# Kernel tuning notes

Measured on AMD Instinct MI355X. Metric: run time of the kernel, lower is better.

Reference implementation:

```python
import jax, jax.numpy as jnp
from jax import lax
import numpy as np

# ---- static configuration (RPN inference path) ----
B = 8
IMG_H, IMG_W = 800, 1216
LEVEL_GRIDS = [(200, 304), (100, 152), (50, 76), (25, 38), (13, 19)]
STRIDES = [4, 8, 16, 32, 64]
SIZES = [32, 64, 128, 256, 512]
RATIOS = np.array([0.5, 1.0, 2.0])
NUM_PER_LEVEL = [h * w * 3 for (h, w) in LEVEL_GRIDS]  # [182400,45600,11400,2850,741]
A_TOTAL = sum(NUM_PER_LEVEL)                            # 242991
PRE_N = 1000   # pre_nms_top_n['testing'], applied per level
POST_N = 1000  # post_nms_top_n['testing']
NMS_THRESH = 0.7
SCORE_THRESH = 0.0
MIN_SIZE = 0.001
BBOX_XFORM_CLIP = float(np.log(1000.0 / 16.0))
LEVEL_OFFSET = 4096.0  # > max image coord, for batched_nms level separation

K_PER_LEVEL = [min(PRE_N, n) for n in NUM_PER_LEVEL]
K_TOTAL = sum(K_PER_LEVEL)  # 4741
LEVELS = jnp.concatenate([jnp.full((k,), i, dtype=jnp.int32)
                          for i, k in enumerate(K_PER_LEVEL)])


def _make_anchors():
    """torchvision-style grid anchors, one scale + 3 aspect ratios per level."""
    all_anchors = []
    for (fh, fw), stride, size in zip(LEVEL_GRIDS, STRIDES, SIZES):
        h_ratios = np.sqrt(RATIOS)
        w_ratios = 1.0 / h_ratios
        ws = w_ratios * size
        hs = h_ratios * size
        base = np.stack([-ws / 2, -hs / 2, ws / 2, hs / 2], axis=1)  # [3,4]
        sx = np.arange(fw, dtype=np.float32) * stride
        sy = np.arange(fh, dtype=np.float32) * stride
        yy, xx = np.meshgrid(sy, sx, indexing='ij')
        shifts = np.stack([xx, yy, xx, yy], axis=-1).reshape(-1, 1, 4)  # [fh*fw,1,4]
        anchors = (shifts + base[None]).reshape(-1, 4)                  # [fh*fw*3,4]
        all_anchors.append(anchors.astype(np.float32))
    return np.concatenate(all_anchors, axis=0)  # [A_TOTAL,4]


def setup_inputs() -> dict:
    key = jax.random.key(0)
    k1, k2 = jax.random.split(key)
    objectness = jax.random.normal(k1, (B, A_TOTAL), dtype=jnp.float32)
    pred_bbox_deltas = jax.random.normal(k2, (B, A_TOTAL, 4), dtype=jnp.float32) * 0.5
    anchors = jnp.asarray(_make_anchors())
    return {"objectness": objectness, "pred_bbox_deltas": pred_bbox_deltas,
            "anchors": anchors}


def _decode(deltas, anchors):
    """BoxCoder.decode with weights (1,1,1,1). deltas [B,A,4], anchors [A,4]."""
    wa = anchors[:, 2] - anchors[:, 0]
    ha = anchors[:, 3] - anchors[:, 1]
    cxa = anchors[:, 0] + 0.5 * wa
    cya = anchors[:, 1] + 0.5 * ha
    dx, dy, dw, dh = deltas[..., 0], deltas[..., 1], deltas[..., 2], deltas[..., 3]
    dw = jnp.minimum(dw, BBOX_XFORM_CLIP)
    dh = jnp.minimum(dh, BBOX_XFORM_CLIP)
    cx = dx * wa + cxa
    cy = dy * ha + cya
    w = jnp.exp(dw) * wa
    h = jnp.exp(dh) * ha
    return jnp.stack([cx - 0.5 * w, cy - 0.5 * h, cx + 0.5 * w, cy + 0.5 * h], axis=-1)


def _per_level_topk(objectness):
    """_get_top_n_idx: per-level top-k with global offsets. Returns [B,K_TOTAL] int32."""
    idxs, offset = [], 0
    for n, k in zip(NUM_PER_LEVEL, K_PER_LEVEL):
        _, ti = lax.top_k(objectness[:, offset:offset + n], k)
        idxs.append(ti + offset)
        offset += n
    return jnp.concatenate(idxs, axis=1)


def _iou(boxes):  # boxes [K,4] -> [K,K]
    area = (boxes[:, 2] - boxes[:, 0]) * (boxes[:, 3] - boxes[:, 1])
    lt = jnp.maximum(boxes[:, None, :2], boxes[None, :, :2])
    rb = jnp.minimum(boxes[:, None, 2:], boxes[None, :, 2:])
    wh = jnp.clip(rb - lt, 0.0)
    inter = wh[..., 0] * wh[..., 1]
    return inter / (area[:, None] + area[None, :] - inter)


def _nms_image(boxes, scores, levels, valid):
    """clip->filter->batched_nms->post_nms_top_n for one image (fixed shapes)."""
    K = boxes.shape[0]
    order = jnp.argsort(-jnp.where(valid, scores, -jnp.inf))
    b = boxes[order]
    s = scores[order]
    v = valid[order]
    lv = levels[order]
    # batched NMS: offset boxes by level so cross-level boxes never overlap
    bb = b + lv.astype(b.dtype)[:, None] * LEVEL_OFFSET
    iou = lax.stop_gradient(_iou(bb))  # keep decisions are non-differentiable
    idxr = jnp.arange(K)

    def body(i, keep):
        sup = (iou[i] > NMS_THRESH) & (idxr > i) & keep[i]
        return keep & ~sup

    keep = lax.fori_loop(0, K, body, v)
    sel = jnp.where(keep, s, -1.0)  # sigmoid scores are > 0
    top_s, top_i = lax.top_k(sel, POST_N)
    kept = top_s > 0.0
    out_b = jnp.where(kept[:, None], b[top_i], 0.0)
    out_s = jnp.where(kept, top_s, 0.0)
    return out_b, out_s


def reference(objectness, pred_bbox_deltas, anchors):
    # box decode for all anchors
    proposals = _decode(pred_bbox_deltas, anchors)          # [B,A,4]
    # per-level topk + gather
    idx = _per_level_topk(objectness)                       # [B,K]
    obj = jnp.take_along_axis(objectness, idx, axis=1)      # [B,K]
    props = jnp.take_along_axis(proposals, idx[..., None], axis=1)  # [B,K,4]
    scores = jax.nn.sigmoid(obj)
    lv = jnp.broadcast_to(LEVELS, idx.shape)
    # clip_boxes_to_image
    x1 = jnp.clip(props[..., 0], 0.0, IMG_W)
    y1 = jnp.clip(props[..., 1], 0.0, IMG_H)
    x2 = jnp.clip(props[..., 2], 0.0, IMG_W)
    y2 = jnp.clip(props[..., 3], 0.0, IMG_H)
    props = jnp.stack([x1, y1, x2, y2], axis=-1)
    # remove_small_boxes + score_thresh
    valid = (x2 - x1 >= MIN_SIZE) & (y2 - y1 >= MIN_SIZE) & (scores >= SCORE_THRESH)
    boxes_out, scores_out = jax.vmap(_nms_image)(props, scores, lv, valid)
    return boxes_out, scores_out  # [B,POST_N,4], [B,POST_N] (zero-padded)
```

## Files before the change

### kernel.cpp

```cpp
#include <hip/hip_runtime.h>
#include <stdint.h>

#pragma clang fp contract(off)

typedef unsigned int u32;
typedef unsigned long long u64;

#define A_TOTAL 242991
#define KTOT    4741

__constant__ int c_LN[5]   = {182400, 45600, 11400, 2850, 741};
__constant__ int c_LOFF[5] = {0, 182400, 228000, 239400, 242250};
__constant__ int c_LK[5]   = {1000, 1000, 1000, 1000, 741};

__constant__ int c_SL[33] = {0,0,0,0,0,0,0,0,0,0,0,0,0,0,0,0,0,0,0,0,0,0,0,
                             1,1,1,1,1,1, 2,2, 3, 4};
__constant__ int c_SS[33] = {0,8192,16384,24576,32768,40960,49152,57344,65536,
                             73728,81920,90112,98304,106496,114688,122880,131072,
                             139264,147456,155648,163840,172032,180224,
                             0,8192,16384,24576,32768,40960, 0,8192, 0, 0};

__constant__ int c_MW[40] = {0,1,2,3, 4,4, 5,5, 6,6, 7,7, 8,8,8, 9,9,9,
                             10,10,10, 11,11,11, 12,12,12,12, 13,13,13,13,
                             14,14,14,14, 15,15,15,15};
__constant__ int c_MR[40] = {0,0,0,0, 0,1, 0,1, 0,1, 0,1, 0,1,2, 0,1,2,
                             0,1,2, 0,1,2, 0,1,2,3, 0,1,2,3,
                             0,1,2,3, 0,1,2,3};

static const size_t OFF_KEEPW    = 0;
static const size_t OFF_HIST     = 0;
static const size_t OFF_SELCNT   = 327680;
static const size_t OFF_CANDCNT  = 327840;
static const size_t MEMSET_BYTES = 328000;
static const size_t OFF_TBIN     = 328000;
static const size_t OFF_CLESS    = 328160;
static const size_t OFF_SELG     = 328320;
static const size_t OFF_CANDG    = 656000;
static const size_t OFF_KEYS     = 1966720;
static const size_t OFF_BOX      = 2270144;
static const size_t OFF_SCORE    = 2876992;
static const size_t OFF_VALID    = 3028704;
static const size_t OFF_MASK     = 3180416;
static const size_t OFF_OUTK     = 8423296;

__device__ __forceinline__ u32 fmap(float f){
  u32 b = __float_as_uint(f);
  return (b & 0x80000000u) ? ~b : (b | 0x80000000u);
}
__device__ __forceinline__ float funmap(u32 m){
  return __uint_as_float((m & 0x80000000u) ? (m & 0x7FFFFFFFu) : ~m);
}

__global__ void __launch_bounds__(1024)
k_hist(const float* __restrict__ obj, u32* __restrict__ hist)
{
  int b = blockIdx.x / 33, s = blockIdx.x % 33;
  int l = c_SL[s], start = c_SS[s];
  int cnt = c_LN[l] - start; if (cnt > 8192) cnt = 8192;
  int bl = b * 5 + l;
  __shared__ u32 h[4][2048];
  for (int i = threadIdx.x; i < 8192; i += 1024) ((u32*)h)[i] = 0;
  __syncthreads();
  u32* hw = h[(threadIdx.x >> 6) & 3];
  const float* p = obj + (size_t)b * A_TOTAL + c_LOFF[l] + start;
  int head = (4 - (int)(((size_t)p >> 2) & 3)) & 3;
  if (head > cnt) head = cnt;
  if ((int)threadIdx.x < head) atomicAdd(&hw[(~fmap(p[threadIdx.x])) >> 21], 1u);
  int nvec = (cnt - head) >> 2;
  const float4* pv = (const float4*)(p + head);
  for (int i = threadIdx.x; i < nvec; i += 1024){
    float4 v = pv[i];
    atomicAdd(&hw[(~fmap(v.x)) >> 21], 1u);
    atomicAdd(&hw[(~fmap(v.y)) >> 21], 1u);
    atomicAdd(&hw[(~fmap(v.z)) >> 21], 1u);
    atomicAdd(&hw[(~fmap(v.w)) >> 21], 1u);
  }
  int tail0 = head + (nvec << 2);
  int ntail = cnt - tail0;
  if ((int)threadIdx.x < ntail) atomicAdd(&hw[(~fmap(p[tail0 + threadIdx.x])) >> 21], 1u);
  __syncthreads();
  for (int i = threadIdx.x; i < 2048; i += 1024){
    u32 v = h[0][i] + h[1][i] + h[2][i] + h[3][i];
    if (v) atomicAdd(&hist[bl * 2048 + i], v);
  }
}

__global__ void __launch_bounds__(256)
k_cutoff(u32* __restrict__ hist, u32* __restrict__ tbin, u32* __restrict__ cless)
{
  int bl = blockIdx.x; int l = bl % 5;
  int K = c_LK[l], n = c_LN[l];
  int tid = threadIdx.x;
  __shared__ u32 cum[2048];
  __shared__ u32 part[256];
  __shared__ int s_t;
  u32 vals[8]; u32 sum = 0;
  for (int q = 0; q < 8; ++q){ vals[q] = hist[bl * 2048 + tid * 8 + q]; sum += vals[q]; }
  part[tid] = sum;
  __syncthreads();
  for (int off = 1; off < 256; off <<= 1){
    u32 add = (tid >= off) ? part[tid - off] : 0u;
    __syncthreads();
    part[tid] += add;
    __syncthreads();
  }
  u32 run = (tid > 0) ? part[tid - 1] : 0u;
  for (int q = 0; q < 8; ++q){ run += vals[q]; cum[tid * 8 + q] = run; }
  __syncthreads();
  if (K >= n){ if (tid == 0){ tbin[bl] = 2048u; cless[bl] = (u32)n; } return; }
  if (tid == 0) s_t = 0;
  __syncthreads();
  for (int q = 0; q < 8; ++q){
    int i = tid * 8 + q;
    u32 c = cum[i], cp = (i > 0) ? cum[i - 1] : 0u;
    if (c >= (u32)K && cp < (u32)K) s_t = i;
  }
  __syncthreads();
  if (tid == 0){
    int t = s_t;
    tbin[bl] = (u32)t;
    cless[bl] = (t > 0) ? cum[t - 1] : 0u;
  }
}

#define SELCAP 2048
#define CANDCAP 1024
__global__ void __launch_bounds__(1024)
k_collect(const float* __restrict__ obj, const u32* __restrict__ tbin,
          u32* __restrict__ selcnt, u32* __restrict__ candcnt,
          u64* __restrict__ selg, u64* __restrict__ candg)
{
  int b = blockIdx.x / 33, s = blockIdx.x % 33;
  int l = c_SL[s], start = c_SS[s];
  int cnt = c_LN[l] - start; if (cnt > 8192) cnt = 8192;
  int bl = b * 5 + l;
  u32 t = tbin[bl];
  __shared__ u64 lsel[SELCAP];
  __shared__ u64 lcand[CANDCAP];
  __shared__ u32 lcs, lcc, gbs, gbc;
  if (threadIdx.x == 0){ lcs = 0u; lcc = 0u; }
  __syncthreads();
  const float* p = obj + (size_t)b * A_TOTAL + c_LOFF[l] + start;

  auto push = [&](u32 m, int idx){
    u32 bin = m >> 21;
    u64 key = ((u64)m << 32) | (u32)idx;
    if (bin < t){
      u32 pos = atomicAdd(&lcs, 1u);
      if (pos < SELCAP) lsel[pos] = key;
      else { u32 gp = atomicAdd(&selcnt[bl], 1u); selg[(size_t)bl * 1024 + gp] = key; }
    } else if (bin == t){
      u32 pos = atomicAdd(&lcc, 1u);
      if (pos < CANDCAP) lcand[pos] = key;
      else { u32 gp = atomicAdd(&candcnt[bl], 1u); if (gp < 4096u) candg[(size_t)bl * 4096 + gp] = key; }
    }
  };

  int head = (4 - (int)(((size_t)p >> 2) & 3)) & 3;
  if (head > cnt) head = cnt;
  if ((int)threadIdx.x < head) push(~fmap(p[threadIdx.x]), start + (int)threadIdx.x);
  int nvec = (cnt - head) >> 2;
  const float4* pv = (const float4*)(p + head);
  for (int i = threadIdx.x; i < nvec; i += 1024){
    float4 v = pv[i];
    int e = start + head + (i << 2);
    push(~fmap(v.x), e);
    push(~fmap(v.y), e + 1);
    push(~fmap(v.z), e + 2);
    push(~fmap(v.w), e + 3);
  }
  int tail0 = head + (nvec << 2);
  int ntail = cnt - tail0;
  if ((int)threadIdx.x < ntail) push(~fmap(p[tail0 + threadIdx.x]), start + tail0 + (int)threadIdx.x);
  __syncthreads();
  u32 ns = lcs;  if (ns > SELCAP) ns = SELCAP;
  u32 ncd = lcc; if (ncd > CANDCAP) ncd = CANDCAP;
  if (threadIdx.x == 0){
    gbs = ns  ? atomicAdd(&selcnt[bl],  ns)  : 0u;
    gbc = ncd ? atomicAdd(&candcnt[bl], ncd) : 0u;
  }
  __syncthreads();
  u32 bs = gbs, bc = gbc;
  for (u32 i = threadIdx.x; i < ns; i += 1024)
    selg[(size_t)bl * 1024 + bs + i] = lsel[i];
  for (u32 i = threadIdx.x; i < ncd; i += 1024){
    u32 gp = bc + i;
    if (gp < 4096u) candg[(size_t)bl * 4096 + gp] = lcand[i];
  }
}

__global__ void __launch_bounds__(1024)
k_select(const u32* __restrict__ selcnt, const u32* __restrict__ candcnt,
         const u64* __restrict__ selg, const u64* __restrict__ candg,
         u64* __restrict__ keys)
{
  int bl = blockIdx.x; int b = bl / 5, l = bl % 5;
  int K = c_LK[l];
  int tid = threadIdx.x;
  __shared__ __align__(16) u64 selU[1024];
  __shared__ __align__(16) u64 candU[4098];
  u32 ns = selcnt[bl]; if (ns > 1024u) ns = 1024u;
  u32 nc = candcnt[bl]; if (nc > 4096u) nc = 4096u;
  int R = K - (int)ns;
  selU[tid] = (tid < (int)ns) ? selg[(size_t)bl * 1024 + tid] : ~0ULL;
  for (u32 i = tid; i < nc; i += 1024) candU[i] = candg[(size_t)bl * 4096 + i];
  u32 nce = (nc + 1u) & ~1u;
  if (tid == 0 && nce > nc) candU[nc] = ~0ULL;
  __syncthreads();
  u64* kout = keys + (size_t)b * KTOT + l * 1000;
  if (tid < (int)ns){
    u64 key = selU[tid];
    u32 r = 0;
    #pragma unroll 8
    for (u32 j = 0; j < 1024; j += 2){
      ulonglong2 v = *reinterpret_cast<const ulonglong2*>(&selU[j]);
      r += (v.x < key) + (v.y < key);
    }
    kout[r] = key;
  }
  if (R > 0){
    for (u32 s = tid; s < nc; s += 1024){
      u64 key = candU[s];
      u32 r = 0;
      #pragma unroll 8
      for (u32 j = 0; j < nce; j += 2){
        ulonglong2 v = *reinterpret_cast<const ulonglong2*>(&candU[j]);
        r += (v.x < key) + (v.y < key);
      }
      if (r < (u32)R) kout[ns + r] = key;
    }
  }
}

__global__ void __launch_bounds__(256)
k_decode(const u64* __restrict__ keys, const float* __restrict__ deltas,
         const float* __restrict__ anchors, float* __restrict__ boxes,
         float* __restrict__ scores, u32* __restrict__ valid)
{
  int g = blockIdx.x * 256 + threadIdx.x;
  if (g >= 8 * KTOT) return;
  int b = g / KTOT, kpos = g % KTOT;
  int l = kpos / 1000; if (l > 4) l = 4;
  u64 key = keys[g];
  u32 idx = (u32)key;
  float o = funmap(~(u32)(key >> 32));
  int ai = c_LOFF[l] + (int)idx;
  const float* a = anchors + (size_t)ai * 4;
  const float* d = deltas + ((size_t)b * A_TOTAL + ai) * 4;
  float a0 = a[0], a1 = a[1], a2 = a[2], a3 = a[3];
  float wa = __fsub_rn(a2, a0), ha = __fsub_rn(a3, a1);
  float cxa = __fadd_rn(a0, __fmul_rn(0.5f, wa));
  float cya = __fadd_rn(a1, __fmul_rn(0.5f, ha));
  float dx = d[0], dy = d[1];
  float dw = fminf(d[2], 4.135166556742356f);
  float dh = fminf(d[3], 4.135166556742356f);
  float cx = __fadd_rn(__fmul_rn(dx, wa), cxa);
  float cy = __fadd_rn(__fmul_rn(dy, ha), cya);
  float w  = __fmul_rn(expf(dw), wa);
  float h  = __fmul_rn(expf(dh), ha);
  float hw = __fmul_rn(0.5f, w), hh = __fmul_rn(0.5f, h);
  float x1 = __fsub_rn(cx, hw), y1 = __fsub_rn(cy, hh);
  float x2 = __fadd_rn(cx, hw), y2 = __fadd_rn(cy, hh);
  x1 = fminf(fmaxf(x1, 0.0f), 1216.0f);
  x2 = fminf(fmaxf(x2, 0.0f), 1216.0f);
  y1 = fminf(fmaxf(y1, 0.0f), 800.0f);
  y2 = fminf(fmaxf(y2, 0.0f), 800.0f);
  float s = __fdiv_rn(1.0f, __fadd_rn(1.0f, expf(-o)));
  int v = (__fsub_rn(x2, x1) >= 0.001f) && (__fsub_rn(y2, y1) >= 0.001f) && (s >= 0.0f);
  float* bo = boxes + (size_t)g * 4;
  bo[0] = x1; bo[1] = y1; bo[2] = x2; bo[3] = y2;
  scores[g] = s;
  valid[g] = (u32)v;
}

__global__ void __launch_bounds__(256)
k_mask(const float* __restrict__ boxes, u64* __restrict__ mask)
{
  int b = blockIdx.x / 184, s = blockIdx.x % 184;
  int l, idx;
  if (s < 160){ l = s / 40; idx = s % 40; }
  else        { l = 4;      idx = s - 160; }
  int w = c_MW[idx], rb = c_MR[idx];
  int N = c_LK[l];
  int koff = l * 1000;
  float offv = (float)(l * 4096);
  __shared__ float sjx1[64], sjy1[64], sjx2[64], sjy2[64], sjar[64];
  int jbase = w * 64;
  if (threadIdx.x < 64){
    int j = jbase + (int)threadIdx.x;
    float x1, y1, x2, y2, ar;
    if (j < N){
      float4 p = ((const float4*)boxes)[(size_t)(b * KTOT + koff + j)];
      x1 = __fadd_rn(p.x, offv); y1 = __fadd_rn(p.y, offv);
      x2 = __fadd_rn(p.z, offv); y2 = __fadd_rn(p.w, offv);
      ar = __fmul_rn(__fsub_rn(x2, x1), __fsub_rn(y2, y1));
    } else {
      x1 = 3e38f; y1 = 3e38f; x2 = -3e38f; y2 = -3e38f; ar = 0.f;
    }
    sjx1[threadIdx.x] = x1; sjy1[threadIdx.x] = y1;
    sjx2[threadIdx.x] = x2; sjy2[threadIdx.x] = y2; sjar[threadIdx.x] = ar;
  }
  __syncthreads();
  int i = rb * 256 + (int)threadIdx.x;
  int rows = (w + 1) * 64; if (rows > N) rows = N;
  if (i >= rows) return;
  float4 p = ((const float4*)boxes)[(size_t)(b * KTOT + koff + i)];
  float bx1 = __fadd_rn(p.x, offv), by1 = __fadd_rn(p.y, offv);
  float bx2 = __fadd_rn(p.z, offv), by2 = __fadd_rn(p.w, offv);
  float bar = __fmul_rn(__fsub_rn(bx2, bx1), __fsub_rn(by2, by1));
  u64 bw = 0;
  #pragma unroll 16
  for (int jj = 0; jj < 64; ++jj){
    int j = jbase + jj;
    float ltx = fmaxf(bx1, sjx1[jj]), lty = fmaxf(by1, sjy1[jj]);
    float rbx = fminf(bx2, sjx2[jj]), rby = fminf(by2, sjy2[jj]);
    float wx = fmaxf(__fsub_rn(rbx, ltx), 0.0f);
    float wy = fmaxf(__fsub_rn(rby, lty), 0.0f);
    float inter = __fmul_rn(wx, wy);
    bool sup = false;
    if (inter > 0.0f && j > i){
      float den = __fsub_rn(__fadd_rn(bar, sjar[jj]), inter);
      sup = __fdiv_rn(inter, den) > 0.7f;
    }
    bw |= ((u64)sup) << jj;
  }
  mask[((size_t)(b * 5 + l) * 16 + w) * 1024 + i] = bw;
}

__global__ void __launch_bounds__(256)
k_nms(const u64* __restrict__ mask, const u32* __restrict__ valid,
      const float* __restrict__ scores, u64* __restrict__ outk,
      u64* __restrict__ keepw)
{
  int bl = blockIdx.x; int b = bl / 5, l = bl % 5;
  int N = c_LK[l], koff = l * 1000;
  int WN = (N + 63) >> 6;
  int tid = threadIdx.x;
  __shared__ u64 s_kw[16];
  __shared__ u64 s_m[7680];
  const u64* mb = mask + (size_t)bl * 16 * 1024;
  int wstage = (WN < 15) ? WN : 15;
  for (int w = 0; w < wstage; ++w){
    int rows = (w + 1) * 64;
    int base = 32 * w * (w + 1);
    for (int r = tid; r < rows; r += 256)
      s_m[base + r] = mb[(size_t)w * 1024 + r];
  }
  __syncthreads();
  if (tid < 64){
    int lane = tid;
    for (int c = 0; c < WN; ++c){
      int i = c * 64 + lane;
      int pred = (i < N) && (valid[(size_t)b * KTOT + koff + i] != 0u);
      u64 bal = __ballot(pred);
      if (lane == 0) s_kw[c] = bal;
    }
    for (int w = 0; w < WN; ++w){
      u64 kwv = s_kw[w];
      u64 supl = 0;
      if (w < 15){
        int base = 32 * w * (w + 1);
        for (int jb = 0; jb < w; ++jb){
          u64 kb = s_kw[jb];
          u64 m = s_m[base + jb * 64 + lane];
          supl |= (((kb >> lane) & 1ULL) ? m : 0ULL);
        }
      } else {
        for (int jb = 0; jb < w; ++jb){
          u64 kb = s_kw[jb];
          u64 m = mb[(size_t)w * 1024 + jb * 64 + lane];
          supl |= (((kb >> lane) & 1ULL) ? m : 0ULL);
        }
      }
      int jr = w * 64 + lane;
      u64 rowl;
      if (w < 15) rowl = s_m[32 * w * (w + 1) + jr];
      else        rowl = (jr < N) ? mb[(size_t)w * 1024 + jr] : 0ULL;
      bool inC = ((kwv >> lane) & 1ULL) != 0ULL;
      u64 rkw = rowl & kwv;
      u64 confl = inC ? rkw : 0ULL;
      u32 a0 = (u32)supl, a1 = (u32)(supl >> 32);
      u32 a2 = (u32)confl, a3 = (u32)(confl >> 32);
      for (int off = 32; off; off >>= 1){
        a0 |= __shfl_xor(a0, off);
        a1 |= __shfl_xor(a1, off);
        a2 |= __shfl_xor(a2, off);
        a3 |= __shfl_xor(a3, off);
      }
      supl = ((u64)a1 << 32) | a0;
      u64 conf = ((u64)a3 << 32) | a2;
      u64 srcb = __ballot(inC && (rkw != 0ULL));
      u64 cur = kwv & ~supl;
      u64 kept = cur;
      if (((srcb & cur) != 0ULL) && ((conf & cur) != 0ULL)){
        u32 rowl_lo = (u32)rowl, rowl_hi = (u32)(rowl >> 32);
        u64 act = cur & (srcb | conf);
        while (act){
          int ib  = __ffsll((unsigned long long)act) - 1;
          int ibs = __builtin_amdgcn_readfirstlane(ib);
          u64 bit = 1ULL << ibs;
          act &= ~bit;
          if (kept & bit){
            u32 rlo = (u32)__builtin_amdgcn_readlane((int)rowl_lo, ibs);
            u32 rhi = (u32)__builtin_amdgcn_readlane((int)rowl_hi, ibs);
            u64 r   = ((u64)rhi << 32) | rlo;
            kept &= ~r;
            act  &= ~r;
          }
        }
      }
      if (lane == 0) s_kw[w] = kept;
    }
  }
  __syncthreads();
  if (tid < 16) keepw[(size_t)bl * 16 + tid] = (tid < WN) ? s_kw[tid] : 0ULL;
  for (int i = tid; i < N; i += 256){
    u64 key = ~0ULL;
    if ((s_kw[i >> 6] >> (i & 63)) & 1ULL){
      float sc = scores[(size_t)b * KTOT + koff + i];
      key = ((u64)(~fmap(sc)) << 32) | (u32)(koff + i);
    }
    outk[(size_t)b * KTOT + koff + i] = key;
  }
}

#define CMPN 1024
__global__ void __launch_bounds__(256)
k_rank(const u64* __restrict__ outk, const u64* __restrict__ keepw,
       const float* __restrict__ boxes, float* __restrict__ out)
{
  int b = blockIdx.x / 19, chunk = blockIdx.x % 19;
  int tid = threadIdx.x;
  __shared__ u64 cmp[5 * CMPN];
  __shared__ u64 kw[80];
  for (int i = tid; i < 5 * CMPN; i += 256) cmp[i] = ~0ULL;
  if (tid < 80) kw[tid] = keepw[(size_t)b * 80 + tid];
  __syncthreads();
  for (int i = tid; i < KTOT; i += 256){
    u64 key = outk[(size_t)b * KTOT + i];
    if (key != ~0ULL){
      int l = i / 1000; if (l > 4) l = 4;
      int li = i - l * 1000;
      int wi = li >> 6, bit = li & 63;
      const u64* kwl = &kw[l * 16];
      int r = __popcll(kwl[wi] & ((1ULL << bit) - 1ULL));
      for (int w = 0; w < wi; ++w) r += __popcll(kwl[w]);
      cmp[l * CMPN + r] = key;
    }
  }
  __syncthreads();
  int i = chunk * 256 + tid;
  if (i >= KTOT) return;
  u64 key = outk[(size_t)b * KTOT + i];
  if (key == ~0ULL) return;
  int l = i / 1000; if (l > 4) l = 4;
  int li = i - l * 1000;
  int wi = li >> 6, bit = li & 63;
  const u64* kwl = &kw[l * 16];
  int rank = __popcll(kwl[wi] & ((1ULL << bit) - 1ULL));
  for (int w = 0; w < wi; ++w) rank += __popcll(kwl[w]);
  #pragma unroll
  for (int lo = 0; lo < 5; ++lo){
    if (lo == l) continue;
    int pos = 0;
    #pragma unroll
    for (int s = 512; s > 0; s >>= 1)
      if (cmp[lo * CMPN + pos + s - 1] < key) pos += s;
    rank += pos;
  }
  if (rank < 1000){
    float4 bx = ((const float4*)boxes)[(size_t)(b * KTOT + i)];
    ((float4*)out)[(size_t)(b * 1000 + rank)] = bx;
    out[32000 + b * 1000 + rank] = funmap(~(u32)(key >> 32));
  }
}

extern "C" void kernel_launch(void* const* d_in, const int* in_sizes, int n_in,
                              void* d_out, int out_size, void* d_ws, size_t ws_size,
                              hipStream_t stream)
{
  (void)in_sizes; (void)n_in; (void)ws_size;
  const float* obj     = (const float*)d_in[0];
  const float* deltas  = (const float*)d_in[1];
  const float* anchors = (const float*)d_in[2];
  float* out = (float*)d_out;
  char* ws = (char*)d_ws;

  u32* hist    = (u32*)(ws + OFF_HIST);
  u64* keepw   = (u64*)(ws + OFF_KEEPW);
  u32* selcnt  = (u32*)(ws + OFF_SELCNT);
  u32* candcnt = (u32*)(ws + OFF_CANDCNT);
  u32* tbin    = (u32*)(ws + OFF_TBIN);
  u32* cless   = (u32*)(ws + OFF_CLESS);
  u64* selg    = (u64*)(ws + OFF_SELG);
  u64* candg   = (u64*)(ws + OFF_CANDG);
  u64* keys    = (u64*)(ws + OFF_KEYS);
  float* boxes = (float*)(ws + OFF_BOX);
  float* score = (float*)(ws + OFF_SCORE);
  u32* valid   = (u32*)(ws + OFF_VALID);
  u64* mask    = (u64*)(ws + OFF_MASK);
  u64* outk    = (u64*)(ws + OFF_OUTK);

  hipMemsetAsync(ws, 0, MEMSET_BYTES, stream);
  hipMemsetAsync(d_out, 0, (size_t)out_size * sizeof(float), stream);
  hipLaunchKernelGGL(k_hist,    dim3(264),  dim3(1024), 0, stream, obj, hist);
  hipLaunchKernelGGL(k_cutoff,  dim3(40),   dim3(256),  0, stream, hist, tbin, cless);
  hipLaunchKernelGGL(k_collect, dim3(264),  dim3(1024), 0, stream, obj, tbin, selcnt, candcnt, selg, candg);
  hipLaunchKernelGGL(k_select,  dim3(40),   dim3(1024), 0, stream, selcnt, candcnt, selg, candg, keys);
  hipLaunchKernelGGL(k_decode,  dim3(149),  dim3(256),  0, stream, keys, deltas, anchors, boxes, score, valid);
  hipLaunchKernelGGL(k_mask,    dim3(1472), dim3(256),  0, stream, boxes, mask);
  hipLaunchKernelGGL(k_nms,     dim3(40),   dim3(256),  0, stream, mask, valid, score, outk, keepw);
  hipLaunchKernelGGL(k_rank,    dim3(152),  dim3(256),  0, stream, outk, keepw, boxes, out);
}
```

Measured before the change: 131.4 us.

## Drop workspace memsets via per-segment histograms and fuse select with decode

The histogram kernel now writes one private histogram per segment with plain stores instead of atomically adding into a zeroed global histogram. The cutoff kernel sums those segments and also zeroes the selection counters and the output buffer, so both hipMemsetAsync calls go away. The top-k select kernel now keeps its sorted keys in shared memory and decodes boxes directly, which removes the separate decode launch and the global keys round trip. The cost is that cutoff reads several segment histograms per level. The keepw region, which the old memset used to clear, is no longer zeroed, so correctness depends on k_nms writing it in full.

After: 144.8 us. 1.1x slower.

```diff
diff --git a/kernel.cpp b/kernel.cpp
--- a/kernel.cpp
+++ b/kernel.cpp
@@ -19,6 +19,8 @@
                              73728,81920,90112,98304,106496,114688,122880,131072,
                              139264,147456,155648,163840,172032,180224,
                              0,8192,16384,24576,32768,40960, 0,8192, 0, 0};
+__constant__ int c_SEG0[5] = {0, 23, 29, 31, 32};
+__constant__ int c_SEGN[5] = {23, 6, 2, 1, 1};
 
 __constant__ int c_MW[40] = {0,1,2,3, 4,4, 5,5, 6,6, 7,7, 8,8,8, 9,9,9,
                              10,10,10, 11,11,11, 12,12,12,12, 13,13,13,13,
@@ -28,20 +30,18 @@
                              0,1,2,3, 0,1,2,3};
 
 static const size_t OFF_KEEPW    = 0;
-static const size_t OFF_HIST     = 0;
 static const size_t OFF_SELCNT   = 327680;
 static const size_t OFF_CANDCNT  = 327840;
-static const size_t MEMSET_BYTES = 328000;
 static const size_t OFF_TBIN     = 328000;
 static const size_t OFF_CLESS    = 328160;
 static const size_t OFF_SELG     = 328320;
 static const size_t OFF_CANDG    = 656000;
-static const size_t OFF_KEYS     = 1966720;
 static const size_t OFF_BOX      = 2270144;
 static const size_t OFF_SCORE    = 2876992;
 static const size_t OFF_VALID    = 3028704;
 static const size_t OFF_MASK     = 3180416;
 static const size_t OFF_OUTK     = 8423296;
+static const size_t OFF_HISTSEG  = 8726720;
 
 __device__ __forceinline__ u32 fmap(float f){
   u32 b = __float_as_uint(f);
@@ -52,12 +52,11 @@
 }
 
 __global__ void __launch_bounds__(1024)
-k_hist(const float* __restrict__ obj, u32* __restrict__ hist)
+k_hist(const float* __restrict__ obj, u32* __restrict__ histseg)
 {
   int b = blockIdx.x / 33, s = blockIdx.x % 33;
   int l = c_SL[s], start = c_SS[s];
   int cnt = c_LN[l] - start; if (cnt > 8192) cnt = 8192;
-  int bl = b * 5 + l;
   __shared__ u32 h[4][2048];
   for (int i = threadIdx.x; i < 8192; i += 1024) ((u32*)h)[i] = 0;
   __syncthreads();
@@ -79,23 +78,31 @@
   int ntail = cnt - tail0;
   if ((int)threadIdx.x < ntail) atomicAdd(&hw[(~fmap(p[tail0 + threadIdx.x])) >> 21], 1u);
   __syncthreads();
-  for (int i = threadIdx.x; i < 2048; i += 1024){
-    u32 v = h[0][i] + h[1][i] + h[2][i] + h[3][i];
-    if (v) atomicAdd(&hist[bl * 2048 + i], v);
-  }
+  u32* hs = histseg + (size_t)(b * 33 + s) * 2048;
+  for (int i = threadIdx.x; i < 2048; i += 1024)
+    hs[i] = h[0][i] + h[1][i] + h[2][i] + h[3][i];
 }
 
 __global__ void __launch_bounds__(256)
-k_cutoff(u32* __restrict__ hist, u32* __restrict__ tbin, u32* __restrict__ cless)
-{
-  int bl = blockIdx.x; int l = bl % 5;
+k_cutoff(const u32* __restrict__ histseg, u32* __restrict__ tbin, u32* __restrict__ cless,
+         u32* __restrict__ selcnt, u32* __restrict__ candcnt, float* __restrict__ out)
+{
+  int bl = blockIdx.x; int b = bl / 5, l = bl % 5;
   int K = c_LK[l], n = c_LN[l];
   int tid = threadIdx.x;
+  if (tid == 0){ selcnt[bl] = 0u; candcnt[bl] = 0u; }
+  for (int i = tid; i < 1000; i += 256) out[bl * 1000 + i] = 0.0f;
   __shared__ u32 cum[2048];
   __shared__ u32 part[256];
   __shared__ int s_t;
+  int s0 = c_SEG0[l], nsg = c_SEGN[l];
   u32 vals[8]; u32 sum = 0;
-  for (int q = 0; q < 8; ++q){ vals[q] = hist[bl * 2048 + tid * 8 + q]; sum += vals[q]; }
+  for (int q = 0; q < 8; ++q){
+    u32 v = 0;
+    for (int k2 = 0; k2 < nsg; ++k2)
+      v += histseg[(size_t)(b * 33 + s0 + k2) * 2048 + tid * 8 + q];
+    vals[q] = v; sum += v;
+  }
   part[tid] = sum;
   __syncthreads();
   for (int off = 1; off < 256; off <<= 1){
@@ -190,15 +197,17 @@
 }
 
 __global__ void __launch_bounds__(1024)
-k_select(const u32* __restrict__ selcnt, const u32* __restrict__ candcnt,
-         const u64* __restrict__ selg, const u64* __restrict__ candg,
-         u64* __restrict__ keys)
+k_selectdec(const u32* __restrict__ selcnt, const u32* __restrict__ candcnt,
+            const u64* __restrict__ selg, const u64* __restrict__ candg,
+            const float* __restrict__ deltas, const float* __restrict__ anchors,
+            float* __restrict__ boxes, float* __restrict__ scores, u32* __restrict__ valid)
 {
   int bl = blockIdx.x; int b = bl / 5, l = bl % 5;
   int K = c_LK[l];
   int tid = threadIdx.x;
   __shared__ __align__(16) u64 selU[1024];
   __shared__ __align__(16) u64 candU[4098];
+  __shared__ u64 keysL[1000];
   u32 ns = selcnt[bl]; if (ns > 1024u) ns = 1024u;
   u32 nc = candcnt[bl]; if (nc > 4096u) nc = 4096u;
   int R = K - (int)ns;
@@ -207,7 +216,6 @@
   u32 nce = (nc + 1u) & ~1u;
   if (tid == 0 && nce > nc) candU[nc] = ~0ULL;
   __syncthreads();
-  u64* kout = keys + (size_t)b * KTOT + l * 1000;
   if (tid < (int)ns){
     u64 key = selU[tid];
     u32 r = 0;
@@ -216,7 +224,7 @@
       ulonglong2 v = *reinterpret_cast<const ulonglong2*>(&selU[j]);
       r += (v.x < key) + (v.y < key);
     }
-    kout[r] = key;
+    keysL[r] = key;
   }
   if (R > 0){
     for (u32 s = tid; s < nc; s += 1024){
@@ -227,50 +235,43 @@
         ulonglong2 v = *reinterpret_cast<const ulonglong2*>(&candU[j]);
         r += (v.x < key) + (v.y < key);
       }
-      if (r < (u32)R) kout[ns + r] = key;
-    }
-  }
-}
-
-__global__ void __launch_bounds__(256)
-k_decode(const u64* __restrict__ keys, const float* __restrict__ deltas,
-         const float* __restrict__ anchors, float* __restrict__ boxes,
-         float* __restrict__ scores, u32* __restrict__ valid)
-{
-  int g = blockIdx.x * 256 + threadIdx.x;
-  if (g >= 8 * KTOT) return;
-  int b = g / KTOT, kpos = g % KTOT;
-  int l = kpos / 1000; if (l > 4) l = 4;
-  u64 key = keys[g];
-  u32 idx = (u32)key;
-  float o = funmap(~(u32)(key >> 32));
-  int ai = c_LOFF[l] + (int)idx;
-  const float* a = anchors + (size_t)ai * 4;
-  const float* d = deltas + ((size_t)b * A_TOTAL + ai) * 4;
-  float a0 = a[0], a1 = a[1], a2 = a[2], a3 = a[3];
-  float wa = __fsub_rn(a2, a0), ha = __fsub_rn(a3, a1);
-  float cxa = __fadd_rn(a0, __fmul_rn(0.5f, wa));
-  float cya = __fadd_rn(a1, __fmul_rn(0.5f, ha));
-  float dx = d[0], dy = d[1];
-  float dw = fminf(d[2], 4.135166556742356f);
-  float dh = fminf(d[3], 4.135166556742356f);
-  float cx = __fadd_rn(__fmul_rn(dx, wa), cxa);
-  float cy = __fadd_rn(__fmul_rn(dy, ha), cya);
-  float w  = __fmul_rn(expf(dw), wa);
-  float h  = __fmul_rn(expf(dh), ha);
-  float hw = __fmul_rn(0.5f, w), hh = __fmul_rn(0.5f, h);
-  float x1 = __fsub_rn(cx, hw), y1 = __fsub_rn(cy, hh);
-  float x2 = __fadd_rn(cx, hw), y2 = __fadd_rn(cy, hh);
-  x1 = fminf(fmaxf(x1, 0.0f), 1216.0f);
-  x2 = fminf(fmaxf(x2, 0.0f), 1216.0f);
-  y1 = fminf(fmaxf(y1, 0.0f), 800.0f);
-  y2 = fminf(fmaxf(y2, 0.0f), 800.0f);
-  float s = __fdiv_rn(1.0f, __fadd_rn(1.0f, expf(-o)));
-  int v = (__fsub_rn(x2, x1) >= 0.001f) && (__fsub_rn(y2, y1) >= 0.001f) && (s >= 0.0f);
-  float* bo = boxes + (size_t)g * 4;
-  bo[0] = x1; bo[1] = y1; bo[2] = x2; bo[3] = y2;
-  scores[g] = s;
-  valid[g] = (u32)v;
+      if (r < (u32)R) keysL[ns + r] = key;
+    }
+  }
+  __syncthreads();
+  if (tid < K){
+    u64 key = keysL[tid];
+    int g = b * KTOT + l * 1000 + tid;
+    u32 idx = (u32)key;
+    float o = funmap(~(u32)(key >> 32));
+    int ai = c_LOFF[l] + (int)idx;
+    const float* a = anchors + (size_t)ai * 4;
+    const float* d = deltas + ((size_t)b * A_TOTAL + ai) * 4;
+    float a0 = a[0], a1 = a[1], a2 = a[2], a3 = a[3];
+    float wa = __fsub_rn(a2, a0), ha = __fsub_rn(a3, a1);
+    float cxa = __fadd_rn(a0, __fmul_rn(0.5f, wa));
+    float cya = __fadd_rn(a1, __fmul_rn(0.5f, ha));
+    float dx = d[0], dy = d[1];
+    float dw = fminf(d[2], 4.135166556742356f);
+    float dh = fminf(d[3], 4.135166556742356f);
+    float cx = __fadd_rn(__fmul_rn(dx, wa), cxa);
+    float cy = __fadd_rn(__fmul_rn(dy, ha), cya);
+    float w  = __fmul_rn(expf(dw), wa);
+    float h  = __fmul_rn(expf(dh), ha);
+    float hw = __fmul_rn(0.5f, w), hh = __fmul_rn(0.5f, h);
+    float x1 = __fsub_rn(cx, hw), y1 = __fsub_rn(cy, hh);
+    float x2 = __fadd_rn(cx, hw), y2 = __fadd_rn(cy, hh);
+    x1 = fminf(fmaxf(x1, 0.0f), 1216.0f);
+    x2 = fminf(fmaxf(x2, 0.0f), 1216.0f);
+    y1 = fminf(fmaxf(y1, 0.0f), 800.0f);
+    y2 = fminf(fmaxf(y2, 0.0f), 800.0f);
+    float s = __fdiv_rn(1.0f, __fadd_rn(1.0f, expf(-o)));
+    int v = (__fsub_rn(x2, x1) >= 0.001f) && (__fsub_rn(y2, y1) >= 0.001f) && (s >= 0.0f);
+    float* bo = boxes + (size_t)g * 4;
+    bo[0] = x1; bo[1] = y1; bo[2] = x2; bo[3] = y2;
+    scores[g] = s;
+    valid[g] = (u32)v;
+  }
 }
 
 __global__ void __launch_bounds__(256)
@@ -479,14 +480,13 @@
                               void* d_out, int out_size, void* d_ws, size_t ws_size,
                               hipStream_t stream)
 {
-  (void)in_sizes; (void)n_in; (void)ws_size;
+  (void)in_sizes; (void)n_in; (void)out_size; (void)ws_size;
   const float* obj     = (const float*)d_in[0];
   const float* deltas  = (const float*)d_in[1];
   const float* anchors = (const float*)d_in[2];
   float* out = (float*)d_out;
   char* ws = (char*)d_ws;
 
-  u32* hist    = (u32*)(ws + OFF_HIST);
   u64* keepw   = (u64*)(ws + OFF_KEEPW);
   u32* selcnt  = (u32*)(ws + OFF_SELCNT);
   u32* candcnt = (u32*)(ws + OFF_CANDCNT);
@@ -494,21 +494,19 @@
   u32* cless   = (u32*)(ws + OFF_CLESS);
   u64* selg    = (u64*)(ws + OFF_SELG);
   u64* candg   = (u64*)(ws + OFF_CANDG);
-  u64* keys    = (u64*)(ws + OFF_KEYS);
   float* boxes = (float*)(ws + OFF_BOX);
   float* score = (float*)(ws + OFF_SCORE);
   u32* valid   = (u32*)(ws + OFF_VALID);
   u64* mask    = (u64*)(ws + OFF_MASK);
   u64* outk    = (u64*)(ws + OFF_OUTK);
-
-  hipMemsetAsync(ws, 0, MEMSET_BYTES, stream);
-  hipMemsetAsync(d_out, 0, (size_t)out_size * sizeof(float), stream);
-  hipLaunchKernelGGL(k_hist,    dim3(264),  dim3(1024), 0, stream, obj, hist);
-  hipLaunchKernelGGL(k_cutoff,  dim3(40),   dim3(256),  0, stream, hist, tbin, cless);
-  hipLaunchKernelGGL(k_collect, dim3(264),  dim3(1024), 0, stream, obj, tbin, selcnt, candcnt, selg, candg);
-  hipLaunchKernelGGL(k_select,  dim3(40),   dim3(1024), 0, stream, selcnt, candcnt, selg, candg, keys);
-  hipLaunchKernelGGL(k_decode,  dim3(149),  dim3(256),  0, stream, keys, deltas, anchors, boxes, score, valid);
-  hipLaunchKernelGGL(k_mask,    dim3(1472), dim3(256),  0, stream, boxes, mask);
-  hipLaunchKernelGGL(k_nms,     dim3(40),   dim3(256),  0, stream, mask, valid, score, outk, keepw);
-  hipLaunchKernelGGL(k_rank,    dim3(152),  dim3(256),  0, stream, outk, keepw, boxes, out);
-}
+  u32* histseg = (u32*)(ws + OFF_HISTSEG);
+
+  hipLaunchKernelGGL(k_hist,      dim3(264),  dim3(1024), 0, stream, obj, histseg);
+  hipLaunchKernelGGL(k_cutoff,    dim3(40),   dim3(256),  0, stream, histseg, tbin, cless, selcnt, candcnt, out);
+  hipLaunchKernelGGL(k_collect,   dim3(264),  dim3(1024), 0, stream, obj, tbin, selcnt, candcnt, selg, candg);
+  hipLaunchKernelGGL(k_selectdec, dim3(40),   dim3(1024), 0, stream, selcnt, candcnt, selg, candg,
+                     deltas, anchors, boxes, score, valid);
+  hipLaunchKernelGGL(k_mask,      dim3(1472), dim3(256),  0, stream, boxes, mask);
+  hipLaunchKernelGGL(k_nms,       dim3(40),   dim3(256),  0, stream, mask, valid, score, outk, keepw);
+  hipLaunchKernelGGL(k_rank,      dim3(152),  dim3(256),  0, stream, outk, keepw, boxes, out);
+}
```
